# Kernel optimization log

Measured on AMD Instinct MI355X. Metric: run time of the kernel, lower is better.

## Reference

```python
import jax, jax.numpy as jnp
import numpy as np

L = 768          # temporal feature length
C_IN = 2048      # feature channels
NA = 10          # anchor scales per position
NC = 21          # num classes (20 + bg)
PRE_NMS = 1024   # pre-NMS top-k
POST_NMS = 128   # fixed proposal count after NMS
NMS_THR = 0.7
SCALE = 1.0      # cfg.Process.new_dilation*new_cluster/Frame
ANCHOR_SIZES = np.array([2., 4., 5., 6., 8., 9., 10., 12., 14., 16.], np.float32)


def _conv(x, w, b, pad=0):
    # x: [N,C,T], w: [O,I,K]
    y = jax.lax.conv_general_dilated(x, w, (1,), [(pad, pad)],
                                     dimension_numbers=('NCH', 'OIH', 'NCH'))
    return y + b[None, :, None]


def _lin(x, w, b):
    return x @ w.T + b


def _forward(feature, p):
    f = _conv(feature, p['w1f'], p['b1f'], 1)
    f = _conv(f, p['w2f'], p['b2f'], 1)
    x = _conv(f, p['wc1'], p['bc1'], 0)                      # [1,512,L]
    # SegmentProposal tower (relu only after conv4, as in source)
    h = _conv(x, p['sp1w'], p['sp1b'], 1)
    h = _conv(h, p['sp2w'], p['sp2b'], 1)
    h = _conv(h, p['sp3w'], p['sp3b'], 1)
    h = jax.nn.relu(_conv(h, p['sp4w'], p['sp4b'], 1))
    cls_score = _conv(h, p['spcw'], p['spcb'], 0)            # [1,2*NA,L]
    seg_pred = _conv(h, p['spsw'], p['spsb'], 0)             # [1,2*NA,L]

    def _resh(t):  # [1,2NA,L] -> [L*NA,2]  (transpose(2,1).view(B,L,C/2,2))
        return jnp.transpose(t, (0, 2, 1)).reshape(-1, 2)

    cls2 = _resh(cls_score)
    cls_prob = jax.nn.softmax(cls2, -1)
    off2 = _resh(seg_pred)

    # anchors: (center, half_len) per position per scale, position-major
    centers = (jnp.arange(L, dtype=jnp.float32) + 0.5) * SCALE
    halves = jnp.asarray(ANCHOR_SIZES) * 0.5
    a_c = jnp.repeat(centers, NA)
    a_h = jnp.tile(halves, L)
    im_info = L * SCALE

    # apply offsets: center shift + log-length scale, clip to video extent
    c = a_c + off2[:, 0] * (2.0 * a_h)
    hl = a_h * jnp.exp(off2[:, 1])
    s = jnp.clip(c - hl, 0.0, im_info)
    e = jnp.clip(c + hl, 0.0, im_info)
    scores = cls_prob[:, 1]

    top_sc, top_i = jax.lax.top_k(scores, PRE_NMS)
    ss, ee = s[top_i], e[top_i]

    def body(i, keep):
        inter = jnp.maximum(0., jnp.minimum(ee, ee[i]) - jnp.maximum(ss, ss[i]))
        union = (ee - ss) + (ee[i] - ss[i]) - inter
        iou = inter / jnp.maximum(union, 1e-8)
        sup = (iou > NMS_THR) & (jnp.arange(PRE_NMS) > i) & keep[i]
        return keep & ~sup

    keep = jax.lax.fori_loop(0, PRE_NMS, body, jnp.ones(PRE_NMS, bool))
    order = jnp.argsort((~keep).astype(jnp.int32), stable=True)  # kept first, score order
    sel = order[:POST_NMS]
    pidx = top_i[sel]
    ps, pe = s[pidx], e[pidx]
    pbbox = jnp.stack([(ps + pe) * 0.5, (pe - ps) * 0.5], -1)    # (center, half)

    # map proposals to feature index range (floor/ceil + clamp, as in source)
    st = jnp.clip(jnp.floor((pbbox[:, 0] - pbbox[:, 1]) / SCALE), 0, L - 1).astype(jnp.int32)
    en = jnp.clip(jnp.ceil((pbbox[:, 0] + pbbox[:, 1]) / SCALE), 0, L - 1).astype(jnp.int32)
    en = jnp.maximum(en, st)

    feat = f[0]                                              # [C_IN, L]
    tpos = jnp.arange(L)
    bins = jnp.arange(7)

    def roi_pool(se):  # AdaptiveMaxPool1d(7) over feat[:, s0:e0+1]
        s0, e0 = se
        ln = e0 - s0 + 1
        bs = s0 + (bins * ln) // 7
        be = s0 + ((bins + 1) * ln + 6) // 7 - 1
        m = (tpos[None, :] >= bs[:, None]) & (tpos[None, :] <= be[:, None])  # [7,L]
        v = jnp.where(m[None], feat[:, None, :], -jnp.inf)   # [C_IN,7,L]
        return v.max(-1)                                     # [C_IN,7]

    spp = jax.lax.map(roi_pool, (st, en))                    # [K,C_IN,7]

    y = _conv(spp, p['wc2'], p['bc2'], 0)
    y = _conv(y, p['w3'], p['b3'], 1)
    y = jax.nn.relu(_conv(y, p['w4'], p['b4'], 1))
    y = _conv(y, p['w5'], p['b5'], 1)
    y = jax.nn.relu(_conv(y, p['w6'], p['b6'], 1))
    y = y.reshape(y.shape[0], -1)                            # [K, 512*7]
    y = _lin(y, p['fc1w'], p['fc1b'])
    # Relation attention is computed but unused in the source forward -> omitted
    y = jax.nn.relu(y)
    y = _lin(y, p['fc2w'], p['fc2b'])
    y = _lin(y, p['fc3w'], p['fc3b'])
    obj_cls = _lin(y, p['clsw'], p['clsb'])                  # [K,NC]
    obj_off = _lin(y, p['boxw'], p['boxb']).reshape(-1, NC - 1, 2)
    cls_sel = cls2[pidx]                                     # [K,2]
    off_sel = off2[pidx]                                     # [K,2]
    return cls_sel, off_sel, obj_cls, obj_off


_PARAM_SHAPES = {
    'w1f': (2048, 2048, 3), 'b1f': (2048,),
    'w2f': (2048, 2048, 3), 'b2f': (2048,),
    'wc1': (512, 2048, 1), 'bc1': (512,),
    'sp1w': (512, 512, 3), 'sp1b': (512,),
    'sp2w': (512, 512, 3), 'sp2b': (512,),
    'sp3w': (512, 512, 3), 'sp3b': (512,),
    'sp4w': (512, 512, 3), 'sp4b': (512,),
    'spcw': (2 * NA, 512, 1), 'spcb': (2 * NA,),
    'spsw': (2 * NA, 512, 1), 'spsb': (2 * NA,),
    'wc2': (512, 2048, 1), 'bc2': (512,),
    'w3': (512, 512, 3), 'b3': (512,),
    'w4': (512, 512, 3), 'b4': (512,),
    'w5': (512, 512, 3), 'b5': (512,),
    'w6': (512, 512, 3), 'b6': (512,),
    'fc1w': (512, 512 * 7), 'fc1b': (512,),
    'fc2w': (256, 512), 'fc2b': (256,),
    'fc3w': (128, 256), 'fc3b': (128,),
    'clsw': (NC, 128), 'clsb': (NC,),
    'boxw': (2 * (NC - 1), 128), 'boxb': (2 * (NC - 1),),
}


def setup_inputs() -> dict:
    key = jax.random.key(0)
    inp = {'feature': jax.random.normal(jax.random.fold_in(key, 0), (1, C_IN, L), jnp.float32)}
    for i, (name, shp) in enumerate(sorted(_PARAM_SHAPES.items())):
        k = jax.random.fold_in(key, i + 1)
        inp[name] = jax.random.normal(k, shp, jnp.float32) * 0.02
    return inp


def reference(feature, b1f, b2f, b3, b4, b5, b6, bc1, bc2, boxb, boxw, clsb, clsw,
              fc1b, fc1w, fc2b, fc2w, fc3b, fc3w, sp1b, sp1w, sp2b, sp2w, sp3b, sp3w,
              sp4b, sp4w, spcb, spcw, spsb, spsw, w1f, w2f, w3, w4, w5, w6,
              wc1, wc2):
    p = dict(w1f=w1f, b1f=b1f, w2f=w2f, b2f=b2f, wc1=wc1, bc1=bc1,
             sp1w=sp1w, sp1b=sp1b, sp2w=sp2w, sp2b=sp2b, sp3w=sp3w, sp3b=sp3b,
             sp4w=sp4w, sp4b=sp4b, spcw=spcw, spcb=spcb, spsw=spsw, spsb=spsb,
             wc2=wc2, bc2=bc2, w3=w3, b3=b3, w4=w4, b4=b4, w5=w5, b5=b5,
             w6=w6, b6=b6, fc1w=fc1w, fc1b=fc1b, fc2w=fc2w, fc2b=fc2b,
             fc3w=fc3w, fc3b=fc3b, clsw=clsw, clsb=clsb, boxw=boxw, boxb=boxb)
    return _forward(feature, p)
```

## Files before the change

### kernel.cpp

```cpp
#include <hip/hip_runtime.h>

typedef __attribute__((ext_vector_type(8))) short short8;
typedef __attribute__((ext_vector_type(4))) float float4v;

__device__ __forceinline__ float bf(unsigned short u) {
    return __uint_as_float(((unsigned int)u) << 16);
}
__device__ __forceinline__ unsigned short f2b(float f) {
    unsigned int u = __float_as_uint(f);
    unsigned int r = (u + 0x7FFFu + ((u >> 16) & 1u)) >> 16;
    return (unsigned short)r;
}

__constant__ float c_anchors[10] = {2.f,4.f,5.f,6.f,8.f,9.f,10.f,12.f,14.f,16.f};

__global__ __launch_bounds__(256) void zeroXt_kernel(unsigned short* __restrict__ Xt, int CI) {
    int i = blockIdx.x * 256 + threadIdx.x;
    if (i < 2 * CI) {
        int row = (i >= CI) ? 769 : 0;
        int co = (i >= CI) ? (i - CI) : i;
        Xt[(size_t)row * CI + co] = 0;
        Xt[(size_t)770 * CI + (size_t)row * CI + co] = 0;
    }
}

__global__ __launch_bounds__(256) void decomp_kernel(const float* __restrict__ src,
                                                     unsigned short* __restrict__ Xt, int CI) {
    __shared__ float T[32][33];
    int l0 = blockIdx.x * 32, ci0 = blockIdx.y * 32;
    int tid = threadIdx.x;
#pragma unroll
    for (int i = 0; i < 4; i++) {
        int slot = tid + 256 * i;
        int r = slot >> 5, c = slot & 31;
        T[r][c] = src[(size_t)(ci0 + r) * 768 + l0 + c];
    }
    __syncthreads();
    unsigned short* Xh = Xt;
    unsigned short* Xl = Xt + (size_t)770 * CI;
#pragma unroll
    for (int i = 0; i < 4; i++) {
        int slot = tid + 256 * i;
        int li = slot >> 5, cc = slot & 31;
        float v = T[cc][li];
        unsigned short h = f2b(v);
        float lo = v - bf(h);
        size_t o = (size_t)(l0 + li + 1) * CI + ci0 + cc;
        Xh[o] = h;
        Xl[o] = f2b(lo);
    }
}

template <int TAPS>
__global__ __launch_bounds__(512, 6) void convmm_kernel(const float* __restrict__ W,
                                                        const unsigned short* __restrict__ Xt,
                                                        float* __restrict__ G,
                                                        int CO, int CI, int S) {
    constexpr int RS = TAPS * 32 + 8;
    __shared__ unsigned short At[2][64 * RS];
    __shared__ unsigned short Bt[2][130 * 40];
    int tid = threadIdx.x;
    int lane = tid & 63, wid = tid >> 6;
    int q = lane >> 4, ln = lane & 15;
    int co0 = blockIdx.x * 64;
    int l0 = blockIdx.y * 128;
    int s = blockIdx.z;
    int kPer = CI / S, cis = s * kPer;
    const unsigned short* Xh = Xt;
    const unsigned short* Xl = Xt + (size_t)770 * CI;

    float4v zero4 = {0.f, 0.f, 0.f, 0.f};
    float4v acc[2][2];
    acc[0][0] = zero4; acc[0][1] = zero4; acc[1][0] = zero4; acc[1][1] = zero4;

    int wave_m = (wid >> 2) * 32;
    int wave_n = (wid & 3) * 32;

    for (int kb = 0; kb < kPer; kb += 32) {
        int cib = cis + kb;
        if (TAPS == 3) {
#pragma unroll
            for (int i = 0; i < 2; i++) {
                int slot = tid + 512 * i;
                int row = slot >> 4, ci0 = (slot & 15) * 2;
                const float* wp = W + ((size_t)(co0 + row) * CI + cib + ci0) * 3;
                float fa[6];
#pragma unroll
                for (int j = 0; j < 6; j++) fa[j] = wp[j];
#pragma unroll
                for (int t = 0; t < 3; t++) {
                    unsigned short h0 = f2b(fa[t]);
                    unsigned short h1 = f2b(fa[t + 3]);
                    unsigned short e0 = f2b(fa[t] - bf(h0));
                    unsigned short e1 = f2b(fa[t + 3] - bf(h1));
                    *(unsigned int*)&At[0][row * RS + t * 32 + ci0] =
                        (unsigned int)h0 | ((unsigned int)h1 << 16);
                    *(unsigned int*)&At[1][row * RS + t * 32 + ci0] =
                        (unsigned int)e0 | ((unsigned int)e1 << 16);
                }
            }
        } else {
            int row = tid >> 3, ci0 = (tid & 7) * 4;
            float4 wv = *(const float4*)(W + (size_t)(co0 + row) * CI + cib + ci0);
            float fa[4] = {wv.x, wv.y, wv.z, wv.w};
            unsigned short h[4], e[4];
#pragma unroll
            for (int j = 0; j < 4; j++) {
                h[j] = f2b(fa[j]);
                e[j] = f2b(fa[j] - bf(h[j]));
            }
            unsigned long long hp = (unsigned long long)h[0] | ((unsigned long long)h[1] << 16) |
                                    ((unsigned long long)h[2] << 32) | ((unsigned long long)h[3] << 48);
            unsigned long long ep = (unsigned long long)e[0] | ((unsigned long long)e[1] << 16) |
                                    ((unsigned long long)e[2] << 32) | ((unsigned long long)e[3] << 48);
            *(unsigned long long*)&At[0][row * RS + ci0] = hp;
            *(unsigned long long*)&At[1][row * RS + ci0] = ep;
        }
#pragma unroll
        for (int i = 0; i < 3; i++) {
            int slot = tid + 512 * i;
            if (slot < 1040) {
                int p = slot >= 520 ? 1 : 0;
                int rem = slot - p * 520;
                int r = rem >> 2, qq = rem & 3;
                const unsigned short* src = (p ? Xl : Xh) + (size_t)(l0 + r) * CI + cib + qq * 8;
                short8 v = *(const short8*)src;
                *(short8*)&Bt[p][r * 40 + qq * 8] = v;
            }
        }
        __syncthreads();
#pragma unroll
        for (int t = 0; t < TAPS; t++) {
            int shift = (TAPS == 1) ? 1 : t;
            short8 bh[2], bl[2];
#pragma unroll
            for (int nf = 0; nf < 2; nf++) {
                int rrow = wave_n + nf * 16 + ln + shift;
                bh[nf] = *(const short8*)&Bt[0][rrow * 40 + q * 8];
                bl[nf] = *(const short8*)&Bt[1][rrow * 40 + q * 8];
            }
#pragma unroll
            for (int mf = 0; mf < 2; mf++) {
                int mrow = wave_m + mf * 16 + ln;
                short8 ah = *(const short8*)&At[0][mrow * RS + t * 32 + q * 8];
                short8 al = *(const short8*)&At[1][mrow * RS + t * 32 + q * 8];
#pragma unroll
                for (int nf = 0; nf < 2; nf++) {
                    acc[mf][nf] = __builtin_amdgcn_mfma_f32_16x16x32_bf16(ah, bh[nf], acc[mf][nf], 0, 0, 0);
                    acc[mf][nf] = __builtin_amdgcn_mfma_f32_16x16x32_bf16(ah, bl[nf], acc[mf][nf], 0, 0, 0);
                    acc[mf][nf] = __builtin_amdgcn_mfma_f32_16x16x32_bf16(al, bh[nf], acc[mf][nf], 0, 0, 0);
                }
            }
        }
        __syncthreads();
    }
    float* Gz = G + (size_t)s * CO * 768;
#pragma unroll
    for (int mf = 0; mf < 2; mf++)
#pragma unroll
        for (int nf = 0; nf < 2; nf++) {
            int col = l0 + wave_n + nf * 16 + ln;
            int rowb = co0 + wave_m + mf * 16 + q * 4;
#pragma unroll
            for (int r = 0; r < 4; r++)
                Gz[(size_t)(rowb + r) * 768 + col] = acc[mf][nf][r];
        }
}

__global__ __launch_bounds__(256) void finsum_x_kernel(const float* __restrict__ G,
                                                       const float* __restrict__ bias,
                                                       unsigned short* __restrict__ Xt,
                                                       int CO, int P) {
    __shared__ float T[64][65];
    int co0 = blockIdx.x * 64, l0 = blockIdx.y * 64;
    int tid = threadIdx.x;
#pragma unroll 1
    for (int i = 0; i < 16; i++) {
        int slot = tid + 256 * i;
        int r = slot >> 6, c = slot & 63;
        float v = bias[co0 + r];
        for (int p = 0; p < P; p++) v += G[((size_t)p * CO + co0 + r) * 768 + l0 + c];
        T[r][c] = v;
    }
    __syncthreads();
    unsigned short* Xh = Xt;
    unsigned short* Xl = Xt + (size_t)770 * CO;
#pragma unroll 1
    for (int i = 0; i < 16; i++) {
        int slot = tid + 256 * i;
        int li = slot >> 6, ci = slot & 63;
        float v = T[ci][li];
        unsigned short h = f2b(v);
        float lo = v - bf(h);
        size_t o = (size_t)(l0 + li + 1) * CO + co0 + ci;
        Xh[o] = h;
        Xl[o] = f2b(lo);
    }
}

__global__ __launch_bounds__(256) void finsum_xf_kernel(const float* __restrict__ G,
                                                        const float* __restrict__ bias,
                                                        unsigned short* __restrict__ Xt,
                                                        float* __restrict__ outF,
                                                        int CO, int P) {
    __shared__ float T[64][65];
    int co0 = blockIdx.x * 64, l0 = blockIdx.y * 64;
    int tid = threadIdx.x;
#pragma unroll 1
    for (int i = 0; i < 16; i++) {
        int slot = tid + 256 * i;
        int r = slot >> 6, c = slot & 63;
        float v = bias[co0 + r];
        for (int p = 0; p < P; p++) v += G[((size_t)p * CO + co0 + r) * 768 + l0 + c];
        T[r][c] = v;
        outF[(size_t)(co0 + r) * 768 + l0 + c] = v;
    }
    __syncthreads();
    unsigned short* Xh = Xt;
    unsigned short* Xl = Xt + (size_t)770 * CO;
#pragma unroll 1
    for (int i = 0; i < 16; i++) {
        int slot = tid + 256 * i;
        int li = slot >> 6, ci = slot & 63;
        float v = T[ci][li];
        unsigned short h = f2b(v);
        float lo = v - bf(h);
        size_t o = (size_t)(l0 + li + 1) * CO + co0 + ci;
        Xh[o] = h;
        Xl[o] = f2b(lo);
    }
}

__global__ __launch_bounds__(256) void finsum_f_kernel(const float* __restrict__ G,
                                                       const float* __restrict__ bias,
                                                       float* __restrict__ out,
                                                       int CO, int P, int relu) {
    int i = blockIdx.x * 256 + threadIdx.x;
    if (i >= CO * 768) return;
    int r = i / 768, c = i - r * 768;
    float v = bias[r];
    for (int p = 0; p < P; p++) v += G[((size_t)p * CO + r) * 768 + c];
    if (relu) v = fmaxf(v, 0.f);
    out[i] = v;
}

__global__ __launch_bounds__(256) void finalize_kernel(const float* __restrict__ part,
                                                       float* __restrict__ out,
                                                       const float* __restrict__ bias,
                                                       int RPAD, int R, int NCOLS, int S, int relu) {
    int i = blockIdx.x * 256 + threadIdx.x;
    int total = R * NCOLS;
    if (i >= total) return;
    int r = i / NCOLS;
    int c = i - r * NCOLS;
    float v = 0.f;
    for (int s = 0; s < S; s++) v += part[((size_t)s * RPAD + r) * NCOLS + c];
    v += bias[r];
    if (relu) v = fmaxf(v, 0.f);
    out[i] = v;
}

template <int MODE, int EPI>
__global__ __launch_bounds__(256) void gemm_kernel(const float* __restrict__ W,
                                                   const float* __restrict__ B,
                                                   const float* __restrict__ bias,
                                                   float* __restrict__ outF,
                                                   int R, int K, int NCOLS, int LDB, int S, int relu) {
    __shared__ __align__(16) float Bt[16][68];
    __shared__ __align__(16) float Wt[16][68];
    int tid = threadIdx.x;
    int tx = tid & 15, ty = tid >> 4;
    int r0 = blockIdx.x * 64, c0 = blockIdx.y * 64, s = blockIdx.z;
    int kPer = K / S;
    int k0s = s * kPer;
    float acc[4][4] = {};
    for (int kb = 0; kb < kPer; kb += 16) {
        int k0 = k0s + kb;
        {
            int rr = r0 + (tid >> 2);
            int q = tid & 3;
            float4 wv4 = {0.f, 0.f, 0.f, 0.f};
            if (rr < R) wv4 = *(const float4*)(W + (size_t)rr * K + k0 + q * 4);
            Wt[q * 4 + 0][tid >> 2] = wv4.x;
            Wt[q * 4 + 1][tid >> 2] = wv4.y;
            Wt[q * 4 + 2][tid >> 2] = wv4.z;
            Wt[q * 4 + 3][tid >> 2] = wv4.w;
        }
#pragma unroll
        for (int p = 0; p < 4; p++) {
            int kk = p * 4 + (tid >> 6);
            int c = tid & 63;
            int k = k0 + kk;
            int col = c0 + c;
            float v;
            if (MODE == 0) {
                v = B[(size_t)k * LDB + col];
            } else if (MODE == 1) {
                int ci = k / 3;
                int t = k - ci * 3;
                int lc = (col % 7) + t - 1;
                v = ((unsigned)lc < 7u) ? B[(size_t)ci * 896 + col + t - 1] : 0.f;
            } else {
                int co = k / 7;
                int b7 = k - co * 7;
                v = B[(size_t)co * 896 + col * 7 + b7];
            }
            Bt[kk][c] = v;
        }
        __syncthreads();
#pragma unroll
        for (int kk = 0; kk < 16; kk++) {
            float4 bv = *(const float4*)&Bt[kk][tx * 4];
            float4 wv = *(const float4*)&Wt[kk][ty * 4];
            float bb[4] = {bv.x, bv.y, bv.z, bv.w};
            float ww[4] = {wv.x, wv.y, wv.z, wv.w};
#pragma unroll
            for (int i = 0; i < 4; i++)
#pragma unroll
                for (int j = 0; j < 4; j++)
                    acc[i][j] = fmaf(ww[i], bb[j], acc[i][j]);
        }
        __syncthreads();
    }
    if (EPI == 0) {
        if (S > 1) {
#pragma unroll
            for (int i = 0; i < 4; i++) {
                int r = r0 + ty * 4 + i;
                float4 o = {acc[i][0], acc[i][1], acc[i][2], acc[i][3]};
                *(float4*)&outF[((size_t)s * R + r) * NCOLS + c0 + tx * 4] = o;
            }
        } else {
#pragma unroll
            for (int i = 0; i < 4; i++) {
                int r = r0 + ty * 4 + i;
                if (r < R) {
                    float bv = bias[r];
#pragma unroll
                    for (int j = 0; j < 4; j++) {
                        float v = acc[i][j] + bv;
                        if (relu) v = fmaxf(v, 0.f);
                        outF[(size_t)r * NCOLS + c0 + tx * 4 + j] = v;
                    }
                }
            }
        }
    } else {
#pragma unroll
        for (int i = 0; i < 4; i++) {
            int r = r0 + ty * 4 + i;
            if (r < R) {
                float bv = bias[r];
#pragma unroll
                for (int j = 0; j < 4; j++) {
                    int col = c0 + tx * 4 + j;
                    float v = acc[i][j] + bv;
                    if (EPI == 1) outF[512 + col * 21 + r] = v;
                    else outF[3200 + col * 40 + r] = v;
                }
            }
        }
    }
}

__global__ __launch_bounds__(256) void proposal_kernel(const float* __restrict__ clsS,
                                                       const float* __restrict__ segS,
                                                       float* __restrict__ cls2, float* __restrict__ off2,
                                                       float* __restrict__ scores,
                                                       float* __restrict__ sArr, float* __restrict__ eArr) {
    int i = blockIdx.x * 256 + threadIdx.x;
    if (i >= 7680) return;
    int l = i / 10;
    int a = i - l * 10;
    float c0 = clsS[(a * 2 + 0) * 768 + l];
    float c1 = clsS[(a * 2 + 1) * 768 + l];
    cls2[i * 2] = c0;
    cls2[i * 2 + 1] = c1;
    float m = fmaxf(c0, c1);
    float e0 = expf(c0 - m), e1 = expf(c1 - m);
    scores[i] = e1 / (e0 + e1);
    float o0 = segS[(a * 2 + 0) * 768 + l];
    float o1 = segS[(a * 2 + 1) * 768 + l];
    off2[i * 2] = o0;
    off2[i * 2 + 1] = o1;
    float ah = c_anchors[a] * 0.5f;
    float ac = (float)l + 0.5f;
    float c = ac + o0 * (2.f * ah);
    float hl = ah * expf(o1);
    sArr[i] = fminf(fmaxf(c - hl, 0.f), 768.f);
    eArr[i] = fminf(fmaxf(c + hl, 0.f), 768.f);
}

__global__ __launch_bounds__(1024) void sortA_kernel(const float* __restrict__ scores,
                                                     unsigned long long* __restrict__ runs) {
    __shared__ unsigned long long kk[1024];
    int tid = threadIdx.x;
    int gbase = blockIdx.x * 1024;
    int gi = gbase + tid;
    unsigned long long key = 0ull;
    if (gi < 7680) {
        unsigned int sb = __float_as_uint(scores[gi]);
        key = ((unsigned long long)sb << 32) | (unsigned long long)(0xFFFFFFFFu - (unsigned)gi);
    }
    kk[tid] = key;
    __syncthreads();
    for (int k = 2; k <= 1024; k <<= 1) {
        for (int j = k >> 1; j > 0; j >>= 1) {
            int ixj = tid ^ j;
            if (ixj > tid) {
                unsigned long long a = kk[tid], b = kk[ixj];
                bool descend = ((tid & k) == 0);
                if (descend ? (a < b) : (a > b)) { kk[tid] = b; kk[ixj] = a; }
            }
            __syncthreads();
        }
    }
    runs[gbase + tid] = kk[tid];
}

__global__ __launch_bounds__(1024) void sortB_kernel(const unsigned long long* __restrict__ runs,
                                                     const float* __restrict__ sArr, const float* __restrict__ eArr,
                                                     int* __restrict__ topI,
                                                     float* __restrict__ ss, float* __restrict__ ee) {
    __shared__ unsigned long long S[8192];
    int tid = threadIdx.x;
#pragma unroll
    for (int m = 0; m < 8; m++) S[m * 1024 + tid] = runs[m * 1024 + tid];
    __syncthreads();
#pragma unroll 1
    for (int level = 0; level < 3; level++) {
        int span = 1024 << level;
        int nm = 4 >> level;
        for (int m = 0; m < nm; m++) {
            int baseA = m * (span * 2);
            int baseB = baseA + span;
            unsigned long long a = S[baseA + tid], b = S[baseB + 1023 - tid];
            S[baseA + tid] = (a > b) ? a : b;
        }
        __syncthreads();
        for (int j = 512; j > 0; j >>= 1) {
            for (int m = 0; m < nm; m++) {
                int baseA = m * (span * 2);
                int ixj = tid ^ j;
                if (ixj > tid) {
                    unsigned long long a = S[baseA + tid], b = S[baseA + ixj];
                    if (a < b) { S[baseA + tid] = b; S[baseA + ixj] = a; }
                }
            }
            __syncthreads();
        }
    }
    int idx = (int)(0xFFFFFFFFu - (unsigned int)(S[tid] & 0xFFFFFFFFull));
    topI[tid] = idx;
    ss[tid] = sArr[idx];
    ee[tid] = eArr[idx];
}

__global__ __launch_bounds__(256) void nms_mask_kernel(const float* __restrict__ ss, const float* __restrict__ ee,
                                                       unsigned long long* __restrict__ mask) {
    int g = blockIdx.x * 256 + threadIdx.x;
    int i = g >> 4, w = g & 15;
    float si = ss[i], ei = ee[i];
    unsigned long long bits = 0ull;
#pragma unroll 1
    for (int jj = 0; jj < 64; jj++) {
        int j = w * 64 + jj;
        if (j > i) {
            float sj = ss[j], ej = ee[j];
            float inter = fmaxf(0.f, fminf(ei, ej) - fmaxf(si, sj));
            float uni = (ej - sj) + (ei - si) - inter;
            float iou = inter / fmaxf(uni, 1e-8f);
            if (iou > 0.7f) bits |= (1ull << jj);
        }
    }
    mask[(size_t)i * 16 + w] = bits;
}

__global__ __launch_bounds__(64) void nms_select_kernel(const unsigned long long* __restrict__ mask,
                                                        const int* __restrict__ topI,
                                                        const float* __restrict__ ss, const float* __restrict__ ee,
                                                        const float* __restrict__ cls2, const float* __restrict__ off2,
                                                        int* __restrict__ stA, int* __restrict__ enA,
                                                        float* __restrict__ out) {
    __shared__ unsigned long long remvS[16];
    __shared__ unsigned long long keepS[16];
    __shared__ int prefixS[17];
    int lane = threadIdx.x;
    if (lane < 16) remvS[lane] = 0ull;
    __syncthreads();
#pragma unroll 1
    for (int b = 0; b < 16; b++) {
        int row = b * 64 + lane;
        const unsigned long long* mrow = mask + (size_t)row * 16;
        unsigned long long diag = mrow[b];
        unsigned long long later[15];
        int nlater = 15 - b;
#pragma unroll 1
        for (int c = 0; c < nlater; c++) later[c] = mrow[b + 1 + c];
        unsigned long long rem = remvS[b];
#pragma unroll 1
        for (int i = 0; i < 64; i++) {
            unsigned long long di = __shfl(diag, i);
            if (!((rem >> i) & 1ull)) rem |= di;
        }
        unsigned long long keep64 = ~rem;
        bool mykeep = (keep64 >> lane) & 1ull;
#pragma unroll 1
        for (int c = 0; c < nlater; c++) {
            unsigned long long v = mykeep ? later[c] : 0ull;
            for (int sft = 1; sft < 64; sft <<= 1) v |= __shfl_xor(v, sft);
            if (lane == 0) remvS[b + 1 + c] |= v;
        }
        if (lane == 0) keepS[b] = keep64;
        __syncthreads();
    }
    if (lane == 0) {
        int acc = 0;
        for (int b = 0; b < 16; b++) { prefixS[b] = acc; acc += __popcll(keepS[b]); }
        prefixS[16] = acc;
    }
    __syncthreads();
    int total = prefixS[16];
#pragma unroll 1
    for (int b = 0; b < 16; b++) {
        int tid = b * 64 + lane;
        unsigned long long keep64 = keepS[b];
        unsigned long long below = (lane == 0) ? 0ull : (keep64 << (64 - lane));
        int keptBefore = prefixS[b] + __popcll(below);
        int kp = (int)((keep64 >> lane) & 1ull);
        int pos = kp ? keptBefore : (total + tid - keptBefore);
        if (pos < 128) {
            int orig = topI[tid];
            float ps = ss[tid], pe = ee[tid];
            out[pos * 2 + 0] = cls2[orig * 2 + 0];
            out[pos * 2 + 1] = cls2[orig * 2 + 1];
            out[256 + pos * 2 + 0] = off2[orig * 2 + 0];
            out[256 + pos * 2 + 1] = off2[orig * 2 + 1];
            float bc = (ps + pe) * 0.5f, bh = (pe - ps) * 0.5f;
            int st = (int)fminf(fmaxf(floorf(bc - bh), 0.f), 767.f);
            int en = (int)fminf(fmaxf(ceilf(bc + bh), 0.f), 767.f);
            if (en < st) en = st;
            stA[pos] = st;
            enA[pos] = en;
        }
    }
}

__global__ __launch_bounds__(256) void roi_kernel(const float* __restrict__ f,
                                                  const int* __restrict__ stA, const int* __restrict__ enA,
                                                  float* __restrict__ spp) {
    int n = blockIdx.x;
    int c = blockIdx.y * 256 + threadIdx.x;
    int st = stA[n], en = enA[n];
    int ln = en - st + 1;
    const float* row = f + (size_t)c * 768;
#pragma unroll 1
    for (int b = 0; b < 7; b++) {
        int bs = st + (b * ln) / 7;
        int be = st + ((b + 1) * ln + 6) / 7 - 1;
        float m = row[bs];
        for (int t = bs + 1; t <= be; t++) m = fmaxf(m, row[t]);
        spp[(size_t)c * 896 + n * 7 + b] = m;
    }
}

extern "C" void kernel_launch(void* const* d_in, const int* in_sizes, int n_in,
                              void* d_out, int out_size, void* d_ws, size_t ws_size,
                              hipStream_t stream) {
    const float* IN[39];
    for (int i = 0; i < 39; i++) IN[i] = (const float*)d_in[i];
    const float* feature = IN[0];
    const float *b1f = IN[1], *b2f = IN[2], *b3 = IN[3], *b4 = IN[4], *b5 = IN[5], *b6 = IN[6];
    const float *bc1 = IN[7], *bc2 = IN[8], *boxb = IN[9], *boxw = IN[10];
    const float *clsb = IN[11], *clsw = IN[12];
    const float *fc1b = IN[13], *fc1w = IN[14], *fc2b = IN[15], *fc2w = IN[16];
    const float *fc3b = IN[17], *fc3w = IN[18];
    const float *sp1b = IN[19], *sp1w = IN[20], *sp2b = IN[21], *sp2w = IN[22];
    const float *sp3b = IN[23], *sp3w = IN[24], *sp4b = IN[25], *sp4w = IN[26];
    const float *spcb = IN[27], *spcw = IN[28], *spsb = IN[29], *spsw = IN[30];
    const float *w1f = IN[31], *w2f = IN[32], *w3w = IN[33], *w4w = IN[34];
    const float *w5w = IN[35], *w6w = IN[36], *wc1 = IN[37], *wc2 = IN[38];
    float* out = (float*)d_out;

    char* base = (char*)d_ws;
    float* G    = (float*)base;
    float* part = (float*)base;
    float* spp  = (float*)(base + 14680064);
    float* yA   = (float*)(base + 22020096);
    float* yB   = (float*)(base + 23855104);
    float* g1   = (float*)(base + 25690112);
    float* g2   = (float*)(base + 25952256);
    float* g3   = (float*)(base + 26083328);
    size_t off = 26148864;
    auto alloc = [&](size_t bytes) { void* p = base + off; off += (bytes + 15) & ~((size_t)15); return p; };
    unsigned short* Xt = (unsigned short*)alloc((size_t)770 * 2048 * 2 * 2);
    float* fbuf = (float*)alloc((size_t)2048 * 768 * 4);
    float* hB   = (float*)alloc((size_t)512 * 768 * 4);
    float* clsS = (float*)alloc((size_t)20 * 768 * 4);
    float* segS = (float*)alloc((size_t)20 * 768 * 4);
    float* cls2 = (float*)alloc(7680 * 2 * 4);
    float* off2 = (float*)alloc(7680 * 2 * 4);
    float* scores = (float*)alloc(7680 * 4);
    float* sArr = (float*)alloc(7680 * 4);
    float* eArr = (float*)alloc(7680 * 4);
    float* ssS  = (float*)alloc(1024 * 4);
    float* eeS  = (float*)alloc(1024 * 4);
    unsigned long long* runs = (unsigned long long*)alloc((size_t)8192 * 8);
    unsigned long long* mask = (unsigned long long*)alloc((size_t)16384 * 8);
    int* topI = (int*)alloc(1024 * 4);
    int* stA = (int*)alloc(128 * 4);
    int* enA = (int*)alloc(128 * 4);

    dim3 blk(256);
    dim3 blk512(512);

    zeroXt_kernel<<<16, blk, 0, stream>>>(Xt, 2048);
    decomp_kernel<<<dim3(24, 64), blk, 0, stream>>>(feature, Xt, 2048);
    convmm_kernel<3><<<dim3(32, 6, 4), blk512, 0, stream>>>(w1f, Xt, G, 2048, 2048, 4);
    finsum_x_kernel<<<dim3(32, 12), blk, 0, stream>>>(G, b1f, Xt, 2048, 4);
    convmm_kernel<3><<<dim3(32, 6, 4), blk512, 0, stream>>>(w2f, Xt, G, 2048, 2048, 4);
    finsum_xf_kernel<<<dim3(32, 12), blk, 0, stream>>>(G, b2f, Xt, fbuf, 2048, 4);

    convmm_kernel<1><<<dim3(8, 6, 8), blk512, 0, stream>>>(wc1, Xt, G, 512, 2048, 8);
    zeroXt_kernel<<<4, blk, 0, stream>>>(Xt, 512);
    finsum_x_kernel<<<dim3(8, 12), blk, 0, stream>>>(G, bc1, Xt, 512, 8);

    convmm_kernel<3><<<dim3(8, 6, 8), blk512, 0, stream>>>(sp1w, Xt, G, 512, 512, 8);
    finsum_x_kernel<<<dim3(8, 12), blk, 0, stream>>>(G, sp1b, Xt, 512, 8);
    convmm_kernel<3><<<dim3(8, 6, 8), blk512, 0, stream>>>(sp2w, Xt, G, 512, 512, 8);
    finsum_x_kernel<<<dim3(8, 12), blk, 0, stream>>>(G, sp2b, Xt, 512, 8);
    convmm_kernel<3><<<dim3(8, 6, 8), blk512, 0, stream>>>(sp3w, Xt, G, 512, 512, 8);
    finsum_x_kernel<<<dim3(8, 12), blk, 0, stream>>>(G, sp3b, Xt, 512, 8);
    convmm_kernel<3><<<dim3(8, 6, 8), blk512, 0, stream>>>(sp4w, Xt, G, 512, 512, 8);
    finsum_f_kernel<<<1536, blk, 0, stream>>>(G, sp4b, hB, 512, 8, 1);

    gemm_kernel<0, 0><<<dim3(1, 12, 1), blk, 0, stream>>>(spcw, hB, spcb, clsS, 20, 512, 768, 768, 1, 0);
    gemm_kernel<0, 0><<<dim3(1, 12, 1), blk, 0, stream>>>(spsw, hB, spsb, segS, 20, 512, 768, 768, 1, 0);

    proposal_kernel<<<30, blk, 0, stream>>>(clsS, segS, cls2, off2, scores, sArr, eArr);
    sortA_kernel<<<8, 1024, 0, stream>>>(scores, runs);
    sortB_kernel<<<1, 1024, 0, stream>>>(runs, sArr, eArr, topI, ssS, eeS);
    nms_mask_kernel<<<64, blk, 0, stream>>>(ssS, eeS, mask);
    nms_select_kernel<<<1, 64, 0, stream>>>(mask, topI, ssS, eeS, cls2, off2, stA, enA, out);

    roi_kernel<<<dim3(128, 8), blk, 0, stream>>>(fbuf, stA, enA, spp);

    gemm_kernel<0, 0><<<dim3(8, 14, 8), blk, 0, stream>>>(wc2, spp, bc2, part, 512, 2048, 896, 896, 8, 0);
    finalize_kernel<<<1792, blk, 0, stream>>>(part, yA, bc2, 512, 512, 896, 8, 0);

    gemm_kernel<1, 0><<<dim3(8, 14, 8), blk, 0, stream>>>(w3w, yA, b3, part, 512, 1536, 896, 896, 8, 0);
    finalize_kernel<<<1792, blk, 0, stream>>>(part, yB, b3, 512, 512, 896, 8, 0);
    gemm_kernel<1, 0><<<dim3(8, 14, 8), blk, 0, stream>>>(w4w, yB, b4, part, 512, 1536, 896, 896, 8, 0);
    finalize_kernel<<<1792, blk, 0, stream>>>(part, yA, b4, 512, 512, 896, 8, 1);
    gemm_kernel<1, 0><<<dim3(8, 14, 8), blk, 0, stream>>>(w5w, yA, b5, part, 512, 1536, 896, 896, 8, 0);
    finalize_kernel<<<1792, blk, 0, stream>>>(part, yB, b5, 512, 512, 896, 8, 0);
    gemm_kernel<1, 0><<<dim3(8, 14, 8), blk, 0, stream>>>(w6w, yB, b6, part, 512, 1536, 896, 896, 8, 0);
    finalize_kernel<<<1792, blk, 0, stream>>>(part, yA, b6, 512, 512, 896, 8, 1);

    gemm_kernel<2, 0><<<dim3(8, 2, 28), blk, 0, stream>>>(fc1w, yA, fc1b, part, 512, 3584, 128, 128, 28, 0);
    finalize_kernel<<<256, blk, 0, stream>>>(part, g1, fc1b, 512, 512, 128, 28, 1);

    gemm_kernel<0, 0><<<dim3(4, 2, 4), blk, 0, stream>>>(fc2w, g1, fc2b, part, 256, 512, 128, 128, 4, 0);
    finalize_kernel<<<128, blk, 0, stream>>>(part, g2, fc2b, 256, 256, 128, 4, 0);
    gemm_kernel<0, 0><<<dim3(2, 2, 2), blk, 0, stream>>>(fc3w, g2, fc3b, part, 128, 256, 128, 128, 2, 0);
    finalize_kernel<<<64, blk, 0, stream>>>(part, g3, fc3b, 128, 128, 128, 2, 0);

    gemm_kernel<0, 1><<<dim3(1, 2, 1), blk, 0, stream>>>(clsw, g3, clsb, out, 21, 128, 128, 128, 1, 0);
    gemm_kernel<0, 2><<<dim3(1, 2, 1), blk, 0, stream>>>(boxw, g3, boxb, out, 40, 128, 128, 128, 1, 0);
}
```

Before: 1.111 ms.

## Restructure NMS select to pull-based suppression with readlane and register state

Rewrites the single-wave NMS selection so each block gathers suppression bits from earlier kept blocks (pull) instead of pushing OR-reductions into shared memory for every later block. Keep masks and prefix sums now live in registers, which removes the shared arrays and __syncthreads. The serial 64-step diagonal scan uses scalar readlane instead of cross-lane shuffles and is fully unrolled. The cost is a dynamically indexed register array, which may spill to scratch, and uncoalesced mask column loads.

```diff
diff --git a/kernel.cpp b/kernel.cpp
--- a/kernel.cpp
+++ b/kernel.cpp
@@ -476,57 +476,50 @@
     mask[(size_t)i * 16 + w] = bits;
 }
 
+__device__ __forceinline__ unsigned long long readlane64(unsigned long long v, int i) {
+    unsigned int lo = (unsigned int)__builtin_amdgcn_readlane((int)(unsigned int)(v & 0xFFFFFFFFull), i);
+    unsigned int hi = (unsigned int)__builtin_amdgcn_readlane((int)(unsigned int)(v >> 32), i);
+    return ((unsigned long long)hi << 32) | (unsigned long long)lo;
+}
+
 __global__ __launch_bounds__(64) void nms_select_kernel(const unsigned long long* __restrict__ mask,
                                                         const int* __restrict__ topI,
                                                         const float* __restrict__ ss, const float* __restrict__ ee,
                                                         const float* __restrict__ cls2, const float* __restrict__ off2,
                                                         int* __restrict__ stA, int* __restrict__ enA,
                                                         float* __restrict__ out) {
-    __shared__ unsigned long long remvS[16];
-    __shared__ unsigned long long keepS[16];
-    __shared__ int prefixS[17];
     int lane = threadIdx.x;
-    if (lane < 16) remvS[lane] = 0ull;
-    __syncthreads();
+    unsigned long long keepW[16];
 #pragma unroll 1
     for (int b = 0; b < 16; b++) {
-        int row = b * 64 + lane;
-        const unsigned long long* mrow = mask + (size_t)row * 16;
-        unsigned long long diag = mrow[b];
-        unsigned long long later[15];
-        int nlater = 15 - b;
-#pragma unroll 1
-        for (int c = 0; c < nlater; c++) later[c] = mrow[b + 1 + c];
-        unsigned long long rem = remvS[b];
-#pragma unroll 1
+        unsigned long long accv = 0ull;
+#pragma unroll 1
+        for (int a = 0; a < b; a++) {
+            unsigned long long m = mask[(size_t)(a * 64 + lane) * 16 + b];
+            unsigned long long kb = (keepW[a] >> lane) & 1ull;
+            accv |= m & (0ull - kb);
+        }
+#pragma unroll
+        for (int sft = 1; sft < 64; sft <<= 1) accv |= __shfl_xor(accv, sft);
+        unsigned long long diag = mask[(size_t)(b * 64 + lane) * 16 + b];
+        unsigned long long rem = accv;
+#pragma unroll
         for (int i = 0; i < 64; i++) {
-            unsigned long long di = __shfl(diag, i);
+            unsigned long long di = readlane64(diag, i);
             if (!((rem >> i) & 1ull)) rem |= di;
         }
-        unsigned long long keep64 = ~rem;
-        bool mykeep = (keep64 >> lane) & 1ull;
-#pragma unroll 1
-        for (int c = 0; c < nlater; c++) {
-            unsigned long long v = mykeep ? later[c] : 0ull;
-            for (int sft = 1; sft < 64; sft <<= 1) v |= __shfl_xor(v, sft);
-            if (lane == 0) remvS[b + 1 + c] |= v;
-        }
-        if (lane == 0) keepS[b] = keep64;
-        __syncthreads();
-    }
-    if (lane == 0) {
-        int acc = 0;
-        for (int b = 0; b < 16; b++) { prefixS[b] = acc; acc += __popcll(keepS[b]); }
-        prefixS[16] = acc;
-    }
-    __syncthreads();
-    int total = prefixS[16];
+        keepW[b] = ~rem;
+    }
+    int total = 0;
+    int prefix[16];
+#pragma unroll
+    for (int b = 0; b < 16; b++) { prefix[b] = total; total += __popcll(keepW[b]); }
 #pragma unroll 1
     for (int b = 0; b < 16; b++) {
         int tid = b * 64 + lane;
-        unsigned long long keep64 = keepS[b];
+        unsigned long long keep64 = keepW[b];
         unsigned long long below = (lane == 0) ? 0ull : (keep64 << (64 - lane));
-        int keptBefore = prefixS[b] + __popcll(below);
+        int keptBefore = prefix[b] + __popcll(below);
         int kp = (int)((keep64 >> lane) & 1ull);
         int pos = kp ? keptBefore : (total + tid - keptBefore);
         if (pos < 128) {
```

Result: faster. 1.065 ms (-4.2%).
